# Optimization experiments

Hardware: AMD Instinct MI355X
Metric: run time of the kernel (lower is better)

## Reference

```python
import jax, jax.numpy as jnp
import numpy as np

EPS = 1e-16
COS_EPS = 1e-8  # torch cosine_similarity clamp


def setup_inputs() -> dict:
    key = jax.random.key(0)
    ks = jax.random.split(key, 9)
    B, N, M = 128, 8192, 64
    return {
        "memory": jax.random.normal(ks[0], (B, N, M), dtype=jnp.float32),
        "k": jax.random.normal(ks[1], (B, M), dtype=jnp.float32),
        "beta": jax.random.uniform(ks[2], (B, 1), dtype=jnp.float32),
        "g": jax.random.uniform(ks[3], (B, 1), dtype=jnp.float32),
        "s": jax.random.uniform(ks[4], (B, 3), dtype=jnp.float32),
        "gamma": jax.random.uniform(ks[5], (B, 1), dtype=jnp.float32),
        "w_prev": jax.random.uniform(ks[6], (B, N), dtype=jnp.float32),
        "e": jax.random.uniform(ks[7], (B, M), dtype=jnp.float32),
        "a": jax.random.normal(ks[8], (B, M), dtype=jnp.float32),
    }


def reference(memory, k, beta, g, s, gamma, w_prev, e, a):
    # --- address (section 3.3) ---
    # content similarity: cosine(memory + eps, k + eps) along feature dim
    mem = memory + EPS                      # [B, N, M]
    kk = k[:, None, :] + EPS                # [B, 1, M]
    dot = jnp.sum(mem * kk, axis=-1)        # [B, N]
    denom = jnp.maximum(
        jnp.linalg.norm(mem, axis=-1) * jnp.linalg.norm(kk, axis=-1), COS_EPS
    )
    w_r = jax.nn.softmax(beta * (dot / denom), axis=1)   # [B, N]
    # interpolate with previous weighting
    w_g = g * w_r + (1.0 - g) * w_prev                   # [B, N]
    # circular shift: conv1d of [w[-1], w, w[0]] with 3-tap kernel s
    # c[i] = w[(i-1)%N]*s0 + w[i]*s1 + w[(i+1)%N]*s2
    shifted = (
        jnp.roll(w_g, 1, axis=1) * s[:, 0:1]
        + w_g * s[:, 1:2]
        + jnp.roll(w_g, -1, axis=1) * s[:, 2:3]
    )                                                     # [B, N]
    # sharpen: w**gamma, renormalize
    w_pow = shifted ** gamma
    w = w_pow / (jnp.sum(w_pow, axis=1, keepdims=True) + EPS)  # [B, N]

    # --- read (section 3.1) ---
    r = jnp.einsum("bn,bnm->bm", w, memory)               # [B, M]

    # --- write (section 3.2): erase then add (rank-1 outer products) ---
    erase = w[:, :, None] * e[:, None, :]                 # [B, N, M]
    add = w[:, :, None] * a[:, None, :]                   # [B, N, M]
    new_memory = memory * (1.0 - erase) + add             # [B, N, M]

    return w, r, new_memory
```

## Files before the change

### kernel.cpp

```cpp
#include <hip/hip_runtime.h>
#include <cmath>


namespace {
constexpr int B = 128;
constexpr int N = 8192;
constexpr int M = 64;
constexpr float F_EPS = 1e-16f;
constexpr float F_COS_EPS = 1e-8f;

constexpr int ROWS = 128;
constexpr int T2 = 512;
constexpr int PER = N / T2;
}

__global__ __launch_bounds__(256) void score_kernel(
    const float* __restrict__ memory, const float* __restrict__ k,
    const float* __restrict__ beta, float* __restrict__ scores)
{
    const int b     = blockIdx.x / (N / ROWS);
    const int chunk = blockIdx.x % (N / ROWS);
    const int wave  = threadIdx.x >> 6;
    const int lane  = threadIdx.x & 63;
    const int grp   = lane >> 4;
    const int m4    = lane & 15;

    const float4 kv = reinterpret_cast<const float4*>(k + (size_t)b * M)[m4];
    const float4 ke = make_float4(kv.x + F_EPS, kv.y + F_EPS,
                                  kv.z + F_EPS, kv.w + F_EPS);
    float kn2 = ke.x*ke.x + ke.y*ke.y + ke.z*ke.z + ke.w*ke.w;
    #pragma unroll
    for (int m = 1; m <= 8; m <<= 1) kn2 += __shfl_xor(kn2, m, 64);
    const float knorm = sqrtf(kn2);
    const float bb = beta[b];

    const int rows_per_wave = ROWS / 4;
    const int row0 = chunk * ROWS + wave * rows_per_wave;

    #pragma unroll 4
    for (int it = 0; it < rows_per_wave; it += 4) {
        const int row = row0 + it + grp;
        const size_t off = ((size_t)b * N + row) * M;
        const float4 mv = reinterpret_cast<const float4*>(memory + off)[m4];
        const float4 me = make_float4(mv.x + F_EPS, mv.y + F_EPS,
                                      mv.z + F_EPS, mv.w + F_EPS);
        float dot = me.x*ke.x + me.y*ke.y + me.z*ke.z + me.w*ke.w;
        float n2  = me.x*me.x + me.y*me.y + me.z*me.z + me.w*me.w;
        #pragma unroll
        for (int m = 1; m <= 8; m <<= 1) {
            dot += __shfl_xor(dot, m, 64);
            n2  += __shfl_xor(n2,  m, 64);
        }
        if (m4 == 0) {
            const float denom = fmaxf(sqrtf(n2) * knorm, F_COS_EPS);
            scores[(size_t)b * N + row] = bb * (dot / denom);
        }
    }
}

__global__ __launch_bounds__(T2) void weight_kernel(
    const float* __restrict__ scores, const float* __restrict__ g,
    const float* __restrict__ s, const float* __restrict__ gamma,
    const float* __restrict__ w_prev, float* __restrict__ w_out,
    float* __restrict__ r_out)
{
    const int b    = blockIdx.x;
    const int tid  = threadIdx.x;
    const int lane = tid & 63;
    const int wave = tid >> 6;

    __shared__ float wg[N];
    __shared__ float red[T2 / 64];

    if (tid < M) r_out[(size_t)b * M + tid] = 0.0f;

    const float* sc = scores + (size_t)b * N;

    float loc[PER];
    float mx = -INFINITY;
    #pragma unroll
    for (int i = 0; i < PER; i++) {
        loc[i] = sc[tid + i * T2];
        mx = fmaxf(mx, loc[i]);
    }
    #pragma unroll
    for (int m = 1; m <= 32; m <<= 1) mx = fmaxf(mx, __shfl_xor(mx, m, 64));
    if (lane == 0) red[wave] = mx;
    __syncthreads();
    float bmx = red[0];
    #pragma unroll
    for (int i = 1; i < T2 / 64; i++) bmx = fmaxf(bmx, red[i]);
    __syncthreads();

    float lsum = 0.0f;
    #pragma unroll
    for (int i = 0; i < PER; i++) {
        loc[i] = expf(loc[i] - bmx);
        lsum += loc[i];
    }
    #pragma unroll
    for (int m = 1; m <= 32; m <<= 1) lsum += __shfl_xor(lsum, m, 64);
    if (lane == 0) red[wave] = lsum;
    __syncthreads();
    float bsum = 0.0f;
    #pragma unroll
    for (int i = 1; i < T2 / 64 + 1; i++) bsum += red[i - 1];
    const float inv = 1.0f / bsum;

    const float gb = g[b];
    #pragma unroll
    for (int i = 0; i < PER; i++) {
        const int idx = tid + i * T2;
        const float wr = loc[i] * inv;
        wg[idx] = gb * wr + (1.0f - gb) * w_prev[(size_t)b * N + idx];
    }
    __syncthreads();

    const float s0 = s[b * 3 + 0], s1 = s[b * 3 + 1], s2 = s[b * 3 + 2];
    const float gm = gamma[b];
    float pv[PER];
    float lsum2 = 0.0f;
    #pragma unroll
    for (int i = 0; i < PER; i++) {
        const int idx = tid + i * T2;
        const float sh = wg[(idx - 1) & (N - 1)] * s0
                       + wg[idx] * s1
                       + wg[(idx + 1) & (N - 1)] * s2;
        pv[i] = powf(sh, gm);
        lsum2 += pv[i];
    }
    #pragma unroll
    for (int m = 1; m <= 32; m <<= 1) lsum2 += __shfl_xor(lsum2, m, 64);
    __syncthreads();
    if (lane == 0) red[wave] = lsum2;
    __syncthreads();
    float bsum2 = 0.0f;
    #pragma unroll
    for (int i = 0; i < T2 / 64; i++) bsum2 += red[i];
    const float invn = 1.0f / (bsum2 + F_EPS);

    #pragma unroll
    for (int i = 0; i < PER; i++) {
        const int idx = tid + i * T2;
        w_out[(size_t)b * N + idx] = pv[i] * invn;
    }
}

__global__ __launch_bounds__(256) void update_kernel(
    const float* __restrict__ memory, const float* __restrict__ e,
    const float* __restrict__ a, const float* __restrict__ w,
    float* __restrict__ newmem, float* __restrict__ r_out)
{
    const int b     = blockIdx.x / (N / ROWS);
    const int chunk = blockIdx.x % (N / ROWS);
    const int wave  = threadIdx.x >> 6;
    const int lane  = threadIdx.x & 63;
    const int grp   = lane >> 4;
    const int m4    = lane & 15;

    const float4 ev = reinterpret_cast<const float4*>(e + (size_t)b * M)[m4];
    const float4 av = reinterpret_cast<const float4*>(a + (size_t)b * M)[m4];

    const int rows_per_wave = ROWS / 4;
    const int row0 = chunk * ROWS + wave * rows_per_wave;

    float4 acc = make_float4(0.f, 0.f, 0.f, 0.f);

    #pragma unroll 4
    for (int it = 0; it < rows_per_wave; it += 4) {
        const int row = row0 + it + grp;
        const size_t off = ((size_t)b * N + row) * M;
        const float4 mv = reinterpret_cast<const float4*>(memory + off)[m4];
        const float ww = w[(size_t)b * N + row];
        float4 nv;
        nv.x = mv.x * (1.0f - ww * ev.x) + ww * av.x;
        nv.y = mv.y * (1.0f - ww * ev.y) + ww * av.y;
        nv.z = mv.z * (1.0f - ww * ev.z) + ww * av.z;
        nv.w = mv.w * (1.0f - ww * ev.w) + ww * av.w;
        reinterpret_cast<float4*>(newmem + off)[m4] = nv;
        acc.x += ww * mv.x;
        acc.y += ww * mv.y;
        acc.z += ww * mv.z;
        acc.w += ww * mv.w;
    }

    #pragma unroll
    for (int m = 16; m <= 32; m <<= 1) {
        acc.x += __shfl_xor(acc.x, m, 64);
        acc.y += __shfl_xor(acc.y, m, 64);
        acc.z += __shfl_xor(acc.z, m, 64);
        acc.w += __shfl_xor(acc.w, m, 64);
    }

    __shared__ float sred[4][M];
    if (grp == 0) {
        sred[wave][m4 * 4 + 0] = acc.x;
        sred[wave][m4 * 4 + 1] = acc.y;
        sred[wave][m4 * 4 + 2] = acc.z;
        sred[wave][m4 * 4 + 3] = acc.w;
    }
    __syncthreads();
    if (threadIdx.x < M) {
        const float v = sred[0][threadIdx.x] + sred[1][threadIdx.x]
                      + sred[2][threadIdx.x] + sred[3][threadIdx.x];
        atomicAdd(&r_out[(size_t)b * M + threadIdx.x], v);
    }
}

extern "C" void kernel_launch(void* const* d_in, const int* in_sizes, int n_in,
                              void* d_out, int out_size, void* d_ws, size_t ws_size,
                              hipStream_t stream) {
    const float* memory = (const float*)d_in[0];
    const float* k      = (const float*)d_in[1];
    const float* beta   = (const float*)d_in[2];
    const float* g      = (const float*)d_in[3];
    const float* s      = (const float*)d_in[4];
    const float* gamma  = (const float*)d_in[5];
    const float* w_prev = (const float*)d_in[6];
    const float* e      = (const float*)d_in[7];
    const float* a      = (const float*)d_in[8];

    float* out    = (float*)d_out;
    float* w_out  = out;
    float* r_out  = out + (size_t)B * N;
    float* newmem = out + (size_t)B * N + (size_t)B * M;

    float* scores = newmem;

    const dim3 blk(256);
    const dim3 grid1(B * (N / ROWS));

    score_kernel<<<grid1, blk, 0, stream>>>(memory, k, beta, scores);
    weight_kernel<<<dim3(B), dim3(T2), 0, stream>>>(scores, g, s, gamma,
                                                    w_prev, w_out, r_out);
    update_kernel<<<grid1, blk, 0, stream>>>(memory, e, a, w_out,
                                             newmem, r_out);
}
```

Baseline: 520.9 us.

## Fuse softmax exp and partial sums into score kernel, drop max pass

The score kernel now writes exp(beta*cos) directly and stores per-chunk partial sums into the r output buffer. The weight kernel sums those partials for normalization instead of running separate max and sum reductions over the scores. It also doubles the weight kernel's block size, and the update kernel uses nontemporal stores for new memory. Dropping the max subtraction assumes beta*cosine stays small enough that exp cannot overflow.

```diff
diff --git a/kernel.cpp b/kernel.cpp
--- a/kernel.cpp
+++ b/kernel.cpp
@@ -10,16 +10,20 @@
 constexpr float F_COS_EPS = 1e-8f;
 
 constexpr int ROWS = 128;
-constexpr int T2 = 512;
+constexpr int CHUNKS = N / ROWS;
+constexpr int T2 = 1024;
 constexpr int PER = N / T2;
 }
+
+typedef float vfloat4 __attribute__((ext_vector_type(4)));
 
 __global__ __launch_bounds__(256) void score_kernel(
     const float* __restrict__ memory, const float* __restrict__ k,
-    const float* __restrict__ beta, float* __restrict__ scores)
+    const float* __restrict__ beta, float* __restrict__ p_out,
+    float* __restrict__ partial)
 {
-    const int b     = blockIdx.x / (N / ROWS);
-    const int chunk = blockIdx.x % (N / ROWS);
+    const int b     = blockIdx.x / CHUNKS;
+    const int chunk = blockIdx.x % CHUNKS;
     const int wave  = threadIdx.x >> 6;
     const int lane  = threadIdx.x & 63;
     const int grp   = lane >> 4;
@@ -36,6 +40,8 @@
 
     const int rows_per_wave = ROWS / 4;
     const int row0 = chunk * ROWS + wave * rows_per_wave;
+
+    float psum = 0.0f;
 
     #pragma unroll 4
     for (int it = 0; it < rows_per_wave; it += 4) {
@@ -53,13 +59,24 @@
         }
         if (m4 == 0) {
             const float denom = fmaxf(sqrtf(n2) * knorm, F_COS_EPS);
-            scores[(size_t)b * N + row] = bb * (dot / denom);
+            const float pe = expf(bb * (dot / denom));
+            p_out[(size_t)b * N + row] = pe;
+            psum += pe;
         }
     }
+
+    psum += __shfl_xor(psum, 16, 64);
+    psum += __shfl_xor(psum, 32, 64);
+
+    __shared__ float ps[4];
+    if (lane == 0) ps[wave] = psum;
+    __syncthreads();
+    if (threadIdx.x == 0)
+        partial[b * CHUNKS + chunk] = ps[0] + ps[1] + ps[2] + ps[3];
 }
 
 __global__ __launch_bounds__(T2) void weight_kernel(
-    const float* __restrict__ scores, const float* __restrict__ g,
+    const float* __restrict__ p, const float* __restrict__ g,
     const float* __restrict__ s, const float* __restrict__ gamma,
     const float* __restrict__ w_prev, float* __restrict__ w_out,
     float* __restrict__ r_out)
@@ -71,47 +88,24 @@
 
     __shared__ float wg[N];
     __shared__ float red[T2 / 64];
+    __shared__ float sS;
+
+    if (tid < 64) {
+        float v = r_out[(size_t)b * M + tid];
+        #pragma unroll
+        for (int m = 1; m <= 32; m <<= 1) v += __shfl_xor(v, m, 64);
+        if (tid == 0) sS = v;
+    }
+    __syncthreads();
+    const float invS = 1.0f / sS;
 
     if (tid < M) r_out[(size_t)b * M + tid] = 0.0f;
-
-    const float* sc = scores + (size_t)b * N;
-
-    float loc[PER];
-    float mx = -INFINITY;
-    #pragma unroll
-    for (int i = 0; i < PER; i++) {
-        loc[i] = sc[tid + i * T2];
-        mx = fmaxf(mx, loc[i]);
-    }
-    #pragma unroll
-    for (int m = 1; m <= 32; m <<= 1) mx = fmaxf(mx, __shfl_xor(mx, m, 64));
-    if (lane == 0) red[wave] = mx;
-    __syncthreads();
-    float bmx = red[0];
-    #pragma unroll
-    for (int i = 1; i < T2 / 64; i++) bmx = fmaxf(bmx, red[i]);
-    __syncthreads();
-
-    float lsum = 0.0f;
-    #pragma unroll
-    for (int i = 0; i < PER; i++) {
-        loc[i] = expf(loc[i] - bmx);
-        lsum += loc[i];
-    }
-    #pragma unroll
-    for (int m = 1; m <= 32; m <<= 1) lsum += __shfl_xor(lsum, m, 64);
-    if (lane == 0) red[wave] = lsum;
-    __syncthreads();
-    float bsum = 0.0f;
-    #pragma unroll
-    for (int i = 1; i < T2 / 64 + 1; i++) bsum += red[i - 1];
-    const float inv = 1.0f / bsum;
 
     const float gb = g[b];
     #pragma unroll
     for (int i = 0; i < PER; i++) {
         const int idx = tid + i * T2;
-        const float wr = loc[i] * inv;
+        const float wr = p[(size_t)b * N + idx] * invS;
         wg[idx] = gb * wr + (1.0f - gb) * w_prev[(size_t)b * N + idx];
     }
     __syncthreads();
@@ -119,7 +113,7 @@
     const float s0 = s[b * 3 + 0], s1 = s[b * 3 + 1], s2 = s[b * 3 + 2];
     const float gm = gamma[b];
     float pv[PER];
-    float lsum2 = 0.0f;
+    float lsum = 0.0f;
     #pragma unroll
     for (int i = 0; i < PER; i++) {
         const int idx = tid + i * T2;
@@ -127,17 +121,16 @@
                        + wg[idx] * s1
                        + wg[(idx + 1) & (N - 1)] * s2;
         pv[i] = powf(sh, gm);
-        lsum2 += pv[i];
-    }
-    #pragma unroll
-    for (int m = 1; m <= 32; m <<= 1) lsum2 += __shfl_xor(lsum2, m, 64);
-    __syncthreads();
-    if (lane == 0) red[wave] = lsum2;
-    __syncthreads();
-    float bsum2 = 0.0f;
-    #pragma unroll
-    for (int i = 0; i < T2 / 64; i++) bsum2 += red[i];
-    const float invn = 1.0f / (bsum2 + F_EPS);
+        lsum += pv[i];
+    }
+    #pragma unroll
+    for (int m = 1; m <= 32; m <<= 1) lsum += __shfl_xor(lsum, m, 64);
+    if (lane == 0) red[wave] = lsum;
+    __syncthreads();
+    float bsum = 0.0f;
+    #pragma unroll
+    for (int i = 0; i < T2 / 64; i++) bsum += red[i];
+    const float invn = 1.0f / (bsum + F_EPS);
 
     #pragma unroll
     for (int i = 0; i < PER; i++) {
@@ -151,8 +144,8 @@
     const float* __restrict__ a, const float* __restrict__ w,
     float* __restrict__ newmem, float* __restrict__ r_out)
 {
-    const int b     = blockIdx.x / (N / ROWS);
-    const int chunk = blockIdx.x % (N / ROWS);
+    const int b     = blockIdx.x / CHUNKS;
+    const int chunk = blockIdx.x % CHUNKS;
     const int wave  = threadIdx.x >> 6;
     const int lane  = threadIdx.x & 63;
     const int grp   = lane >> 4;
@@ -172,12 +165,12 @@
         const size_t off = ((size_t)b * N + row) * M;
         const float4 mv = reinterpret_cast<const float4*>(memory + off)[m4];
         const float ww = w[(size_t)b * N + row];
-        float4 nv;
+        vfloat4 nv;
         nv.x = mv.x * (1.0f - ww * ev.x) + ww * av.x;
         nv.y = mv.y * (1.0f - ww * ev.y) + ww * av.y;
         nv.z = mv.z * (1.0f - ww * ev.z) + ww * av.z;
         nv.w = mv.w * (1.0f - ww * ev.w) + ww * av.w;
-        reinterpret_cast<float4*>(newmem + off)[m4] = nv;
+        __builtin_nontemporal_store(nv, (vfloat4*)(newmem + off) + m4);
         acc.x += ww * mv.x;
         acc.y += ww * mv.y;
         acc.z += ww * mv.z;
@@ -225,13 +218,14 @@
     float* r_out  = out + (size_t)B * N;
     float* newmem = out + (size_t)B * N + (size_t)B * M;
 
-    float* scores = newmem;
+    float* p      = newmem;
+    float* partsum = r_out;
 
     const dim3 blk(256);
-    const dim3 grid1(B * (N / ROWS));
-
-    score_kernel<<<grid1, blk, 0, stream>>>(memory, k, beta, scores);
-    weight_kernel<<<dim3(B), dim3(T2), 0, stream>>>(scores, g, s, gamma,
+    const dim3 grid1(B * CHUNKS);
+
+    score_kernel<<<grid1, blk, 0, stream>>>(memory, k, beta, p, partsum);
+    weight_kernel<<<dim3(B), dim3(T2), 0, stream>>>(p, g, s, gamma,
                                                     w_prev, w_out, r_out);
     update_kernel<<<grid1, blk, 0, stream>>>(memory, e, a, w_out,
                                              newmem, r_out);
```

Measured after the change: 507.0 us. 1.03x faster.
